# Kernel optimization log

Hardware: AMD Instinct MI355X
Metric: run time of the kernel (lower is better)

Reference implementation:

```python
import jax, jax.numpy as jnp
import numpy as np
import math

N = 100000
E = 3200000
LAMDA = 0.5
ALPHA = 0.1
NLAYERS = 8


def setup_inputs() -> dict:
    key = jax.random.key(0)
    ks = jax.random.split(key, 9)
    x = jax.random.normal(ks[0], (N, 500), dtype=jnp.float32)
    row = jax.random.randint(ks[1], (E,), 0, N, dtype=jnp.int32)
    col = jax.random.randint(ks[2], (E,), 0, N, dtype=jnp.int32)
    # roughly degree-normalized positive edge weights
    edge_weight = jax.random.uniform(ks[3], (E,), dtype=jnp.float32) * (2.0 / 32.0)
    W_in = jax.random.normal(ks[4], (500, 64), dtype=jnp.float32) * (1.0 / math.sqrt(500.0))
    b_in = jnp.zeros((64,), dtype=jnp.float32)
    conv_W = jax.random.normal(ks[5], (NLAYERS, 64, 64), dtype=jnp.float32) * (1.0 / 8.0)
    W_out = jax.random.normal(ks[6], (64, 40), dtype=jnp.float32) * (1.0 / 8.0)
    b_out = jnp.zeros((40,), dtype=jnp.float32)
    return {"x": x, "row": row, "col": col, "edge_weight": edge_weight,
            "W_in": W_in, "b_in": b_in, "conv_W": conv_W,
            "W_out": W_out, "b_out": b_out}


def _spmm(row, col, w, h):
    # adj @ h with adj in COO form: gather source rows, scatter-add to dest
    msgs = h[col] * w[:, None]            # [E, nhidden]
    return jax.ops.segment_sum(msgs, row, num_segments=N)


def reference(x, row, col, edge_weight, W_in, b_in, conv_W, W_out, b_out):
    # dropout is identity in eval mode
    h0 = jax.nn.relu(x @ W_in + b_in)     # [N, nhidden]
    h = h0
    for i in range(NLAYERS):
        l = i + 1
        beta = math.log(LAMDA / l + 1.0)  # identity-mapping strength
        hi = _spmm(row, col, edge_weight, h)
        support = (1.0 - ALPHA) * hi + ALPHA * h0   # initial residual
        h = jax.nn.relu(beta * (support @ conv_W[i]) + (1.0 - beta) * support)
    logits = h @ W_out + b_out
    return jax.nn.log_softmax(logits, axis=1)
```

## Files before the change

### kernel.cpp

```cpp
#include <hip/hip_runtime.h>
#include <math.h>

#define FIN 500
#define NHID 64
#define NCLS 40
#define NLAYERS 8
#define CSHIFT 9
#define CROWS (1 << CSHIFT)
#define PTILE 16384

typedef _Float16 half8 __attribute__((ext_vector_type(8)));
typedef float f32x4 __attribute__((ext_vector_type(4)));

__global__ __launch_bounds__(256) void k_prep(
    const float* __restrict__ Wi, const float* __restrict__ Wc,
    _Float16* __restrict__ WtIn, _Float16* __restrict__ WcT) {
  const int t = blockIdx.x * 256 + threadIdx.x;
  const int stride = gridDim.x * 256;
  for (int i = t; i < 64 * 512; i += stride) {
    int c = i >> 9, k = i & 511;
    WtIn[i] = (k < FIN) ? (_Float16)Wi[k * 64 + c] : (_Float16)0.f;
  }
  for (int i = t; i < NLAYERS * 64 * 64; i += stride) {
    int l = i >> 12, rem = i & 4095, c = rem >> 6, k = rem & 63;
    WcT[i] = (_Float16)Wc[l * 4096 + k * 64 + c];
  }
}

__device__ __forceinline__ half8 load_a_frag(const float* __restrict__ xrow, int gk) {
  half8 a;
  if (gk + 7 < FIN) {
    float4 u = *reinterpret_cast<const float4*>(xrow + gk);
    float4 v = *reinterpret_cast<const float4*>(xrow + gk + 4);
    a[0] = (_Float16)u.x; a[1] = (_Float16)u.y;
    a[2] = (_Float16)u.z; a[3] = (_Float16)u.w;
    a[4] = (_Float16)v.x; a[5] = (_Float16)v.y;
    a[6] = (_Float16)v.z; a[7] = (_Float16)v.w;
  } else {
#pragma unroll
    for (int j = 0; j < 8; ++j)
      a[j] = (gk + j < FIN) ? (_Float16)xrow[gk + j] : (_Float16)0.f;
  }
  return a;
}

__global__ __launch_bounds__(256) void k_gemm_in(
    const float* __restrict__ x, const _Float16* __restrict__ Wt,
    const float* __restrict__ b, _Float16* __restrict__ h0, int n) {
  const int lane = threadIdx.x & 63;
  const int wv = threadIdx.x >> 6;
  const int row0 = blockIdx.x * 64 + wv * 16;
  const int arow = row0 + (lane & 15);
  const int gr = (arow < n) ? arow : (n - 1);
  const int kg = (lane >> 4) * 8;
  const float* xrow = x + (size_t)gr * FIN;
  f32x4 acc[4];
#pragma unroll
  for (int ct = 0; ct < 4; ++ct) acc[ct] = (f32x4){0.f, 0.f, 0.f, 0.f};
  half8 a = load_a_frag(xrow, kg);
#pragma unroll 2
  for (int k0 = 0; k0 < 512; k0 += 32) {
    half8 an = a;
    if (k0 + 32 < 512) an = load_a_frag(xrow, k0 + 32 + kg);
#pragma unroll
    for (int ct = 0; ct < 4; ++ct) {
      const half8 bf = *reinterpret_cast<const half8*>(
          Wt + (size_t)(ct * 16 + (lane & 15)) * 512 + k0 + kg);
      acc[ct] = __builtin_amdgcn_mfma_f32_16x16x32_f16(a, bf, acc[ct], 0, 0, 0);
    }
    a = an;
  }
  const int orow = row0 + (lane >> 4) * 4;
#pragma unroll
  for (int ct = 0; ct < 4; ++ct) {
    const int c = ct * 16 + (lane & 15);
    const float bb = b[c];
#pragma unroll
    for (int i = 0; i < 4; ++i) {
      const int rr = orow + i;
      if (rr < n)
        h0[(size_t)rr * NHID + c] = (_Float16)fmaxf(acc[ct][i] + bb, 0.f);
    }
  }
}

__global__ __launch_bounds__(256) void k_chist(
    const int* __restrict__ row, int* __restrict__ ccnt, int e_total) {
  __shared__ int hist[256];
  const int tid = threadIdx.x;
  hist[tid] = 0;
  __syncthreads();
  const int e0 = blockIdx.x * PTILE;
  for (int t = 0; t < PTILE / 256; ++t) {
    int e = e0 + t * 256 + tid;
    if (e < e_total) atomicAdd(&hist[row[e] >> CSHIFT], 1);
  }
  __syncthreads();
  if (hist[tid]) atomicAdd(&ccnt[tid], hist[tid]);
}

__global__ __launch_bounds__(256) void k_cscan(
    const int* __restrict__ ccnt, int* __restrict__ cbase,
    int* __restrict__ bcur, int* __restrict__ ptr, int nbC, int n, int E) {
  __shared__ int sh[257];
  const int t = threadIdx.x;
  sh[t] = (t < nbC) ? ccnt[t] : 0;
  __syncthreads();
  if (t == 0) {
    int run = 0;
    for (int i = 0; i < 256; ++i) { int v = sh[i]; sh[i] = run; run += v; }
    sh[256] = run;
  }
  __syncthreads();
  if (t <= nbC) cbase[t] = sh[t];
  if (t < nbC) bcur[t] = sh[t];
  if (t == 0) ptr[n] = E;
}

__global__ __launch_bounds__(256) void k_part2(
    const int* __restrict__ row, const int* __restrict__ col,
    const float* __restrict__ w, int* __restrict__ bcurG,
    int2* __restrict__ staged, int e_total, int nbC) {
  __shared__ int hist[256];
  __shared__ int cur[256];
  const int tid = threadIdx.x;
  const int e0 = blockIdx.x * PTILE;
  if (tid < nbC) hist[tid] = 0;
  __syncthreads();
  for (int t = 0; t < PTILE / 256; ++t) {
    int e = e0 + t * 256 + tid;
    if (e < e_total) atomicAdd(&hist[row[e] >> CSHIFT], 1);
  }
  __syncthreads();
  if (tid < nbC) {
    int h = hist[tid];
    cur[tid] = h ? atomicAdd(&bcurG[tid], h) : 0;
  }
  __syncthreads();
  for (int t = 0; t < PTILE / 256; ++t) {
    int e = e0 + t * 256 + tid;
    if (e < e_total) {
      int r = row[e];
      int pos = atomicAdd(&cur[r >> CSHIFT], 1);
      staged[pos] = make_int2(((r & (CROWS - 1)) << 17) | col[e], __float_as_int(w[e]));
    }
  }
}

__global__ __launch_bounds__(256) void k_rebin3(
    const int* __restrict__ cbase, const int2* __restrict__ staged,
    int2* __restrict__ sorted, int* __restrict__ ptr, int n) {
  __shared__ int rcnt[CROWS];
  __shared__ int cur[CROWS];
  __shared__ int wsum[4];
  const int tid = threadIdx.x;
  const int r0 = blockIdx.x << CSHIFT;
  const int bstart = cbase[blockIdx.x], bend = cbase[blockIdx.x + 1];
  rcnt[tid] = 0; rcnt[tid + 256] = 0;
  __syncthreads();
  for (int i = bstart + tid; i < bend; i += 256)
    atomicAdd(&rcnt[staged[i].x >> 17], 1);
  __syncthreads();
  const int lane = tid & 63, wid = tid >> 6;
  int v0 = rcnt[2 * tid], v1 = rcnt[2 * tid + 1];
  int s = v0 + v1;
  int incl = s;
#pragma unroll
  for (int off = 1; off < 64; off <<= 1) {
    int u = __shfl_up(incl, off, 64);
    if (lane >= off) incl += u;
  }
  if (lane == 63) wsum[wid] = incl;
  __syncthreads();
  int woff = 0;
  for (int i = 0; i < wid; ++i) woff += wsum[i];
  int base = bstart + incl - s + woff;
  int rr = r0 + 2 * tid;
  if (rr < n) ptr[rr] = base;
  if (rr + 1 < n) ptr[rr + 1] = base + v0;
  cur[2 * tid] = base;
  cur[2 * tid + 1] = base + v0;
  __syncthreads();
  for (int i = bstart + tid; i < bend; i += 256) {
    int2 e = staged[i];
    int pos = atomicAdd(&cur[e.x >> 17], 1);
    sorted[pos] = make_int2(e.x & 0x1FFFF, e.y);
  }
}

__global__ __launch_bounds__(256) void k_spmm_csr(
    const int* __restrict__ ptr, const int2* __restrict__ sorted,
    const half8* __restrict__ hh, const half8* __restrict__ h0h,
    half8* __restrict__ Sh, int n, int wstride) {
  const int lane = threadIdx.x & 63;
  const int sub = lane >> 3;
  const int fl = lane & 7;
  for (int r = blockIdx.x * 4 + (threadIdx.x >> 6); r < n; r += wstride) {
    const int start = ptr[r], end = ptr[r + 1];
    const half8 h0v = h0h[(size_t)r * 8 + fl];
    float acc[8] = {};
    int e = start + sub;
    for (; e + 24 < end; e += 32) {
      const int2 c0 = sorted[e];
      const int2 c1 = sorted[e + 8];
      const int2 c2 = sorted[e + 16];
      const int2 c3 = sorted[e + 24];
      const half8 v0 = hh[(size_t)c0.x * 8 + fl];
      const half8 v1 = hh[(size_t)c1.x * 8 + fl];
      const half8 v2 = hh[(size_t)c2.x * 8 + fl];
      const half8 v3 = hh[(size_t)c3.x * 8 + fl];
      const float w0 = __int_as_float(c0.y);
      const float w1 = __int_as_float(c1.y);
      const float w2 = __int_as_float(c2.y);
      const float w3 = __int_as_float(c3.y);
#pragma unroll
      for (int j = 0; j < 8; ++j)
        acc[j] += w0 * (float)v0[j] + w1 * (float)v1[j] +
                  w2 * (float)v2[j] + w3 * (float)v3[j];
    }
    for (; e < end; e += 8) {
      const int2 cw = sorted[e];
      const float wv = __int_as_float(cw.y);
      const half8 hv = hh[(size_t)cw.x * 8 + fl];
#pragma unroll
      for (int j = 0; j < 8; ++j) acc[j] += wv * (float)hv[j];
    }
#pragma unroll
    for (int off = 8; off < 64; off <<= 1)
#pragma unroll
      for (int j = 0; j < 8; ++j) acc[j] += __shfl_xor(acc[j], off, 64);
    if (sub == 0) {
      half8 o;
#pragma unroll
      for (int j = 0; j < 8; ++j)
        o[j] = (_Float16)(0.9f * acc[j] + 0.1f * (float)h0v[j]);
      Sh[(size_t)r * 8 + fl] = o;
    }
  }
}

__global__ __launch_bounds__(256) void k_layer(
    const _Float16* __restrict__ Sh, const _Float16* __restrict__ Wt,
    _Float16* __restrict__ hout, float beta, int n) {
  const int lane = threadIdx.x & 63;
  const int wv = threadIdx.x >> 6;
  const int row0 = blockIdx.x * 64 + wv * 16;
  const int arow = row0 + (lane & 15);
  const int gr = (arow < n) ? arow : (n - 1);
  const int kg = (lane >> 4) * 8;
  const half8 a0 = *reinterpret_cast<const half8*>(Sh + (size_t)gr * NHID + kg);
  const half8 a1 = *reinterpret_cast<const half8*>(Sh + (size_t)gr * NHID + 32 + kg);
  f32x4 acc[4];
#pragma unroll
  for (int ct = 0; ct < 4; ++ct) acc[ct] = (f32x4){0.f, 0.f, 0.f, 0.f};
#pragma unroll
  for (int ct = 0; ct < 4; ++ct) {
    const int c = ct * 16 + (lane & 15);
    const half8 b0 = *reinterpret_cast<const half8*>(Wt + c * NHID + kg);
    const half8 b1 = *reinterpret_cast<const half8*>(Wt + c * NHID + 32 + kg);
    acc[ct] = __builtin_amdgcn_mfma_f32_16x16x32_f16(a0, b0, acc[ct], 0, 0, 0);
    acc[ct] = __builtin_amdgcn_mfma_f32_16x16x32_f16(a1, b1, acc[ct], 0, 0, 0);
  }
  const float g = 1.f - beta;
  const int orow = row0 + (lane >> 4) * 4;
#pragma unroll
  for (int ct = 0; ct < 4; ++ct) {
    const int c = ct * 16 + (lane & 15);
#pragma unroll
    for (int i = 0; i < 4; ++i) {
      const int rr = orow + i;
      if (rr < n) {
        const float s = (float)Sh[(size_t)rr * NHID + c];
        hout[(size_t)rr * NHID + c] =
            (_Float16)fmaxf(beta * acc[ct][i] + g * s, 0.f);
      }
    }
  }
}

__global__ __launch_bounds__(256) void k_out(
    const _Float16* __restrict__ h, const float* __restrict__ Wo,
    const float* __restrict__ bo, float* __restrict__ out, int n, int wstride) {
  const int lane = threadIdx.x & 63;
  const int j = (lane < NCLS) ? lane : (NCLS - 1);
  for (int r = blockIdx.x * 4 + (threadIdx.x >> 6); r < n; r += wstride) {
    const float hv = (float)h[(size_t)r * NHID + lane];
    float acc = bo[j];
#pragma unroll 16
    for (int k = 0; k < NHID; ++k) {
      float hk = __shfl(hv, k, 64);
      acc += hk * Wo[k * NCLS + j];
    }
    float v = (lane < NCLS) ? acc : -INFINITY;
    float m = v;
#pragma unroll
    for (int off = 32; off; off >>= 1) m = fmaxf(m, __shfl_xor(m, off, 64));
    float e = (lane < NCLS) ? expf(acc - m) : 0.f;
    float s = e;
#pragma unroll
    for (int off = 32; off; off >>= 1) s += __shfl_xor(s, off, 64);
    if (lane < NCLS) out[(size_t)r * NCLS + lane] = acc - m - logf(s);
  }
}

extern "C" void kernel_launch(void* const* d_in, const int* in_sizes, int n_in,
                              void* d_out, int out_size, void* d_ws, size_t ws_size,
                              hipStream_t stream) {
  const float* x  = (const float*)d_in[0];
  const int* row  = (const int*)d_in[1];
  const int* col  = (const int*)d_in[2];
  const float* ew = (const float*)d_in[3];
  const float* Wi = (const float*)d_in[4];
  const float* bi = (const float*)d_in[5];
  const float* Wc = (const float*)d_in[6];
  const float* Wo = (const float*)d_in[7];
  const float* bo = (const float*)d_in[8];
  float* out = (float*)d_out;

  const int n = in_sizes[0] / FIN;
  const int E = in_sizes[1];

  half8* h0h   = (half8*)d_ws;
  half8* hhA   = h0h + (size_t)n * 8;
  half8* hhB   = hhA + (size_t)n * 8;
  half8* Sh    = hhB + (size_t)n * 8;
  float* A     = (float*)(Sh + (size_t)n * 8);
  int2*  staged= (int2*)A;
  _Float16* WtIn = (_Float16*)A;
  _Float16* WcT  = WtIn + 64 * 512;
  int2*  sorted= (int2*)(A + (size_t)n * NHID);
  int*   ptr   = (int*)(sorted + E);
  int*   ccnt  = ptr + (n + 1);
  int*   cbase = ccnt + 256;
  int*   bcur  = cbase + 257;

  const int nbC = (n + CROWS - 1) >> CSHIFT;
  const int nPB = (E + PTILE - 1) / PTILE;
  dim3 blk(256);

  hipMemsetAsync(ccnt, 0, 256 * sizeof(int), stream);
  k_chist<<<dim3(nPB), blk, 0, stream>>>(row, ccnt, E);
  k_cscan<<<dim3(1), blk, 0, stream>>>(ccnt, cbase, bcur, ptr, nbC, n, E);
  k_part2<<<dim3(nPB), blk, 0, stream>>>(row, col, ew, bcur, staged, E, nbC);
  k_rebin3<<<dim3(nbC), blk, 0, stream>>>(cbase, staged, sorted, ptr, n);

  k_prep<<<dim3(64), blk, 0, stream>>>(Wi, Wc, WtIn, WcT);

  k_gemm_in<<<dim3((n + 63) / 64), blk, 0, stream>>>(x, WtIn, bi, (_Float16*)h0h, n);

  const int spmmBlocks = 2048;
  const half8* hin = h0h;
  for (int l = 0; l < NLAYERS; ++l) {
    half8* hout = (l & 1) ? hhB : hhA;
    k_spmm_csr<<<dim3(spmmBlocks), blk, 0, stream>>>(
        ptr, sorted, hin, h0h, Sh, n, spmmBlocks * 4);
    float beta = logf(0.5f / (float)(l + 1) + 1.f);
    k_layer<<<dim3((n + 63) / 64), blk, 0, stream>>>(
        (const _Float16*)Sh, WcT + (size_t)l * NHID * NHID, (_Float16*)hout, beta, n);
    hin = hout;
  }
  const int outBlocks = 2048;
  k_out<<<dim3(outBlocks), blk, 0, stream>>>(
      (const _Float16*)hin, Wo, bo, out, n, outBlocks * 4);
}
```

Measured before the change: 1.345 ms.

## Fuse SpMM with layer GEMM using column-chunked CSR for cache locality

The edge list is now bucketed by source-column chunk (7 chunks) as well as by destination row block, giving one CSR row-pointer array per chunk. A single fused kernel per layer walks the chunks in turn, accumulates each output row's SpMM result in LDS, adds the initial residual, and runs the MFMA layer transform directly. This removes the intermediate support buffer's global write and read, and the extra kernel launch per layer. It also confines each chunk's gather to a smaller slice of h that is more likely to stay in cache. The cost is that each wave now processes edges one at a time with a scalar fp16 load per lane, instead of eight edges in parallel with vector loads. That adds latency and extra row-pointer reads per chunk.

```diff
diff --git a/kernel.cpp b/kernel.cpp
--- a/kernel.cpp
+++ b/kernel.cpp
@@ -5,9 +5,11 @@
 #define NHID 64
 #define NCLS 40
 #define NLAYERS 8
-#define CSHIFT 9
-#define CROWS (1 << CSHIFT)
 #define PTILE 16384
+#define RSHIFT 12
+#define RROWS 4096
+#define NCHUNK 7
+#define CHSHIFT 14
 
 typedef _Float16 half8 __attribute__((ext_vector_type(8)));
 typedef float f32x4 __attribute__((ext_vector_type(4)));
@@ -85,7 +87,8 @@
 }
 
 __global__ __launch_bounds__(256) void k_chist(
-    const int* __restrict__ row, int* __restrict__ ccnt, int e_total) {
+    const int* __restrict__ row, const int* __restrict__ col,
+    int* __restrict__ ccnt, int e_total, int rh) {
   __shared__ int hist[256];
   const int tid = threadIdx.x;
   hist[tid] = 0;
@@ -93,7 +96,10 @@
   const int e0 = blockIdx.x * PTILE;
   for (int t = 0; t < PTILE / 256; ++t) {
     int e = e0 + t * 256 + tid;
-    if (e < e_total) atomicAdd(&hist[row[e] >> CSHIFT], 1);
+    if (e < e_total) {
+      int ch = col[e] >> CHSHIFT; if (ch > NCHUNK - 1) ch = NCHUNK - 1;
+      atomicAdd(&hist[ch * rh + (row[e] >> RSHIFT)], 1);
+    }
   }
   __syncthreads();
   if (hist[tid]) atomicAdd(&ccnt[tid], hist[tid]);
@@ -101,7 +107,7 @@
 
 __global__ __launch_bounds__(256) void k_cscan(
     const int* __restrict__ ccnt, int* __restrict__ cbase,
-    int* __restrict__ bcur, int* __restrict__ ptr, int nbC, int n, int E) {
+    int* __restrict__ bcur, int nbC) {
   __shared__ int sh[257];
   const int t = threadIdx.x;
   sh[t] = (t < nbC) ? ccnt[t] : 0;
@@ -114,13 +120,12 @@
   __syncthreads();
   if (t <= nbC) cbase[t] = sh[t];
   if (t < nbC) bcur[t] = sh[t];
-  if (t == 0) ptr[n] = E;
 }
 
 __global__ __launch_bounds__(256) void k_part2(
     const int* __restrict__ row, const int* __restrict__ col,
     const float* __restrict__ w, int* __restrict__ bcurG,
-    int2* __restrict__ staged, int e_total, int nbC) {
+    int2* __restrict__ staged, int e_total, int nbC, int rh) {
   __shared__ int hist[256];
   __shared__ int cur[256];
   const int tid = threadIdx.x;
@@ -129,7 +134,10 @@
   __syncthreads();
   for (int t = 0; t < PTILE / 256; ++t) {
     int e = e0 + t * 256 + tid;
-    if (e < e_total) atomicAdd(&hist[row[e] >> CSHIFT], 1);
+    if (e < e_total) {
+      int ch = col[e] >> CHSHIFT; if (ch > NCHUNK - 1) ch = NCHUNK - 1;
+      atomicAdd(&hist[ch * rh + (row[e] >> RSHIFT)], 1);
+    }
   }
   __syncthreads();
   if (tid < nbC) {
@@ -140,30 +148,34 @@
   for (int t = 0; t < PTILE / 256; ++t) {
     int e = e0 + t * 256 + tid;
     if (e < e_total) {
-      int r = row[e];
-      int pos = atomicAdd(&cur[r >> CSHIFT], 1);
-      staged[pos] = make_int2(((r & (CROWS - 1)) << 17) | col[e], __float_as_int(w[e]));
-    }
-  }
-}
-
-__global__ __launch_bounds__(256) void k_rebin3(
+      int r = row[e], c = col[e];
+      int ch = c >> CHSHIFT; if (ch > NCHUNK - 1) ch = NCHUNK - 1;
+      int pos = atomicAdd(&cur[ch * rh + (r >> RSHIFT)], 1);
+      staged[pos] = make_int2(((r & (RROWS - 1)) << 17) | c, __float_as_int(w[e]));
+    }
+  }
+}
+
+__global__ __launch_bounds__(256) void k_rebin4(
     const int* __restrict__ cbase, const int2* __restrict__ staged,
-    int2* __restrict__ sorted, int* __restrict__ ptr, int n) {
-  __shared__ int rcnt[CROWS];
-  __shared__ int cur[CROWS];
+    int2* __restrict__ sorted, int* __restrict__ ptr2, int rh) {
+  __shared__ int rcnt[RROWS];
+  __shared__ int cur[RROWS];
   __shared__ int wsum[4];
   const int tid = threadIdx.x;
-  const int r0 = blockIdx.x << CSHIFT;
+  const int k = blockIdx.x / rh;
+  const int rhigh = blockIdx.x - k * rh;
   const int bstart = cbase[blockIdx.x], bend = cbase[blockIdx.x + 1];
-  rcnt[tid] = 0; rcnt[tid + 256] = 0;
+  for (int i = tid; i < RROWS; i += 256) rcnt[i] = 0;
   __syncthreads();
   for (int i = bstart + tid; i < bend; i += 256)
     atomicAdd(&rcnt[staged[i].x >> 17], 1);
   __syncthreads();
+  const int base = tid * 16;
+  int s = 0;
+#pragma unroll
+  for (int j = 0; j < 16; ++j) s += rcnt[base + j];
   const int lane = tid & 63, wid = tid >> 6;
-  int v0 = rcnt[2 * tid], v1 = rcnt[2 * tid + 1];
-  int s = v0 + v1;
   int incl = s;
 #pragma unroll
   for (int off = 1; off < 64; off <<= 1) {
@@ -174,12 +186,15 @@
   __syncthreads();
   int woff = 0;
   for (int i = 0; i < wid; ++i) woff += wsum[i];
-  int base = bstart + incl - s + woff;
-  int rr = r0 + 2 * tid;
-  if (rr < n) ptr[rr] = base;
-  if (rr + 1 < n) ptr[rr + 1] = base + v0;
-  cur[2 * tid] = base;
-  cur[2 * tid + 1] = base + v0;
+  int run = bstart + (incl - s) + woff;
+  int* p2 = ptr2 + (size_t)k * (rh << RSHIFT) + (rhigh << RSHIFT);
+#pragma unroll
+  for (int j = 0; j < 16; ++j) {
+    int c = rcnt[base + j];
+    p2[base + j] = run;
+    cur[base + j] = run;
+    run += c;
+  }
   __syncthreads();
   for (int i = bstart + tid; i < bend; i += 256) {
     int2 e = staged[i];
@@ -188,91 +203,87 @@
   }
 }
 
-__global__ __launch_bounds__(256) void k_spmm_csr(
-    const int* __restrict__ ptr, const int2* __restrict__ sorted,
-    const half8* __restrict__ hh, const half8* __restrict__ h0h,
-    half8* __restrict__ Sh, int n, int wstride) {
-  const int lane = threadIdx.x & 63;
-  const int sub = lane >> 3;
-  const int fl = lane & 7;
-  for (int r = blockIdx.x * 4 + (threadIdx.x >> 6); r < n; r += wstride) {
-    const int start = ptr[r], end = ptr[r + 1];
-    const half8 h0v = h0h[(size_t)r * 8 + fl];
-    float acc[8] = {};
-    int e = start + sub;
-    for (; e + 24 < end; e += 32) {
-      const int2 c0 = sorted[e];
-      const int2 c1 = sorted[e + 8];
-      const int2 c2 = sorted[e + 16];
-      const int2 c3 = sorted[e + 24];
-      const half8 v0 = hh[(size_t)c0.x * 8 + fl];
-      const half8 v1 = hh[(size_t)c1.x * 8 + fl];
-      const half8 v2 = hh[(size_t)c2.x * 8 + fl];
-      const half8 v3 = hh[(size_t)c3.x * 8 + fl];
-      const float w0 = __int_as_float(c0.y);
-      const float w1 = __int_as_float(c1.y);
-      const float w2 = __int_as_float(c2.y);
-      const float w3 = __int_as_float(c3.y);
-#pragma unroll
-      for (int j = 0; j < 8; ++j)
-        acc[j] += w0 * (float)v0[j] + w1 * (float)v1[j] +
-                  w2 * (float)v2[j] + w3 * (float)v3[j];
-    }
-    for (; e < end; e += 8) {
-      const int2 cw = sorted[e];
-      const float wv = __int_as_float(cw.y);
-      const half8 hv = hh[(size_t)cw.x * 8 + fl];
-#pragma unroll
-      for (int j = 0; j < 8; ++j) acc[j] += wv * (float)hv[j];
-    }
-#pragma unroll
-    for (int off = 8; off < 64; off <<= 1)
-#pragma unroll
-      for (int j = 0; j < 8; ++j) acc[j] += __shfl_xor(acc[j], off, 64);
-    if (sub == 0) {
-      half8 o;
-#pragma unroll
-      for (int j = 0; j < 8; ++j)
-        o[j] = (_Float16)(0.9f * acc[j] + 0.1f * (float)h0v[j]);
-      Sh[(size_t)r * 8 + fl] = o;
-    }
-  }
-}
-
-__global__ __launch_bounds__(256) void k_layer(
-    const _Float16* __restrict__ Sh, const _Float16* __restrict__ Wt,
-    _Float16* __restrict__ hout, float beta, int n) {
-  const int lane = threadIdx.x & 63;
-  const int wv = threadIdx.x >> 6;
-  const int row0 = blockIdx.x * 64 + wv * 16;
-  const int arow = row0 + (lane & 15);
-  const int gr = (arow < n) ? arow : (n - 1);
+__global__ __launch_bounds__(256, 8) void k_fused(
+    const int* __restrict__ ptr2, const int2* __restrict__ sorted,
+    const _Float16* __restrict__ hin, const _Float16* __restrict__ h0,
+    const _Float16* __restrict__ Wt, _Float16* __restrict__ hout,
+    float beta, int n, int s2) {
+  __shared__ float S[64 * 66];
+  const int tid = threadIdx.x;
+  const int lane = tid & 63;
+  const int wid = tid >> 6;
+  const int row0 = blockIdx.x * 64;
+  for (int i = tid; i < 64 * 66; i += 256) S[i] = 0.f;
+  __syncthreads();
+  const int rbase = row0 + wid * 16;
+  const _Float16* hl = hin + lane;
+  for (int k = 0; k < NCHUNK; ++k) {
+    const int* p2 = ptr2 + (size_t)k * s2;
+    int e0 = p2[rbase];
+    for (int rr = 0; rr < 16; ++rr) {
+      const int r = rbase + rr;
+      if (r >= n) break;
+      const int e1 = p2[r + 1];
+      float acc = 0.f;
+      int e = e0;
+      for (; e + 3 < e1; e += 4) {
+        const int2 c0 = sorted[e];
+        const int2 c1 = sorted[e + 1];
+        const int2 c2 = sorted[e + 2];
+        const int2 c3 = sorted[e + 3];
+        const float v0 = (float)hl[(size_t)c0.x * NHID];
+        const float v1 = (float)hl[(size_t)c1.x * NHID];
+        const float v2 = (float)hl[(size_t)c2.x * NHID];
+        const float v3 = (float)hl[(size_t)c3.x * NHID];
+        acc += __int_as_float(c0.y) * v0 + __int_as_float(c1.y) * v1 +
+               __int_as_float(c2.y) * v2 + __int_as_float(c3.y) * v3;
+      }
+      for (; e < e1; ++e) {
+        const int2 cw = sorted[e];
+        acc += __int_as_float(cw.y) * (float)hl[(size_t)cw.x * NHID];
+      }
+      S[(wid * 16 + rr) * 66 + lane] += acc;
+      e0 = e1;
+    }
+  }
+  for (int rr = 0; rr < 16; ++rr) {
+    const int r = rbase + rr;
+    if (r >= n) break;
+    float* sp = &S[(wid * 16 + rr) * 66 + lane];
+    *sp = 0.9f * *sp + 0.1f * (float)h0[(size_t)r * NHID + lane];
+  }
+  __syncthreads();
+  const int al = lane & 15;
   const int kg = (lane >> 4) * 8;
-  const half8 a0 = *reinterpret_cast<const half8*>(Sh + (size_t)gr * NHID + kg);
-  const half8 a1 = *reinterpret_cast<const half8*>(Sh + (size_t)gr * NHID + 32 + kg);
+  const float* sa = &S[(wid * 16 + al) * 66 + kg];
+  half8 a0, a1;
+#pragma unroll
+  for (int j = 0; j < 8; ++j) a0[j] = (_Float16)sa[j];
+#pragma unroll
+  for (int j = 0; j < 8; ++j) a1[j] = (_Float16)sa[32 + j];
   f32x4 acc[4];
 #pragma unroll
   for (int ct = 0; ct < 4; ++ct) acc[ct] = (f32x4){0.f, 0.f, 0.f, 0.f};
 #pragma unroll
   for (int ct = 0; ct < 4; ++ct) {
-    const int c = ct * 16 + (lane & 15);
+    const int c = ct * 16 + al;
     const half8 b0 = *reinterpret_cast<const half8*>(Wt + c * NHID + kg);
     const half8 b1 = *reinterpret_cast<const half8*>(Wt + c * NHID + 32 + kg);
     acc[ct] = __builtin_amdgcn_mfma_f32_16x16x32_f16(a0, b0, acc[ct], 0, 0, 0);
     acc[ct] = __builtin_amdgcn_mfma_f32_16x16x32_f16(a1, b1, acc[ct], 0, 0, 0);
   }
   const float g = 1.f - beta;
-  const int orow = row0 + (lane >> 4) * 4;
+  const int ri = (lane >> 4) * 4;
 #pragma unroll
   for (int ct = 0; ct < 4; ++ct) {
-    const int c = ct * 16 + (lane & 15);
+    const int c = ct * 16 + al;
 #pragma unroll
     for (int i = 0; i < 4; ++i) {
-      const int rr = orow + i;
-      if (rr < n) {
-        const float s = (float)Sh[(size_t)rr * NHID + c];
-        hout[(size_t)rr * NHID + c] =
-            (_Float16)fmaxf(beta * acc[ct][i] + g * s, 0.f);
+      const int r = rbase + ri + i;
+      if (r < n) {
+        const float sv = S[(wid * 16 + ri + i) * 66 + c];
+        hout[(size_t)r * NHID + c] =
+            (_Float16)fmaxf(beta * acc[ct][i] + g * sv, 0.f);
       }
     }
   }
@@ -320,46 +331,44 @@
   const int n = in_sizes[0] / FIN;
   const int E = in_sizes[1];
 
-  half8* h0h   = (half8*)d_ws;
-  half8* hhA   = h0h + (size_t)n * 8;
-  half8* hhB   = hhA + (size_t)n * 8;
-  half8* Sh    = hhB + (size_t)n * 8;
-  float* A     = (float*)(Sh + (size_t)n * 8);
-  int2*  staged= (int2*)A;
-  _Float16* WtIn = (_Float16*)A;
+  const int rh = (n + RROWS - 1) >> RSHIFT;
+  const int s2 = rh << RSHIFT;
+  const int nbC2 = NCHUNK * rh;
+
+  _Float16* h0h = (_Float16*)d_ws;
+  _Float16* hhA = h0h + (size_t)n * NHID;
+  _Float16* hhB = hhA + (size_t)n * NHID;
+  int2* staged  = (int2*)(hhB + (size_t)n * NHID);
+  int2* sorted  = staged + E;
+  int*  ptr2    = (int*)(sorted + E);
+  int*  ccnt    = ptr2 + (size_t)NCHUNK * s2 + 1;
+  int*  cbase   = ccnt + 256;
+  int*  bcur    = cbase + 257;
+  _Float16* WtIn = (_Float16*)(((uintptr_t)(bcur + 256) + 63) & ~(uintptr_t)63);
   _Float16* WcT  = WtIn + 64 * 512;
-  int2*  sorted= (int2*)(A + (size_t)n * NHID);
-  int*   ptr   = (int*)(sorted + E);
-  int*   ccnt  = ptr + (n + 1);
-  int*   cbase = ccnt + 256;
-  int*   bcur  = cbase + 257;
-
-  const int nbC = (n + CROWS - 1) >> CSHIFT;
+
   const int nPB = (E + PTILE - 1) / PTILE;
+  const int nBF = (n + 63) / 64;
   dim3 blk(256);
 
   hipMemsetAsync(ccnt, 0, 256 * sizeof(int), stream);
-  k_chist<<<dim3(nPB), blk, 0, stream>>>(row, ccnt, E);
-  k_cscan<<<dim3(1), blk, 0, stream>>>(ccnt, cbase, bcur, ptr, nbC, n, E);
-  k_part2<<<dim3(nPB), blk, 0, stream>>>(row, col, ew, bcur, staged, E, nbC);
-  k_rebin3<<<dim3(nbC), blk, 0, stream>>>(cbase, staged, sorted, ptr, n);
+  k_chist<<<dim3(nPB), blk, 0, stream>>>(row, col, ccnt, E, rh);
+  k_cscan<<<dim3(1), blk, 0, stream>>>(ccnt, cbase, bcur, nbC2);
+  k_part2<<<dim3(nPB), blk, 0, stream>>>(row, col, ew, bcur, staged, E, nbC2, rh);
+  k_rebin4<<<dim3(nbC2), blk, 0, stream>>>(cbase, staged, sorted, ptr2, rh);
 
   k_prep<<<dim3(64), blk, 0, stream>>>(Wi, Wc, WtIn, WcT);
 
-  k_gemm_in<<<dim3((n + 63) / 64), blk, 0, stream>>>(x, WtIn, bi, (_Float16*)h0h, n);
-
-  const int spmmBlocks = 2048;
-  const half8* hin = h0h;
+  k_gemm_in<<<dim3(nBF), blk, 0, stream>>>(x, WtIn, bi, h0h, n);
+
+  const _Float16* hin = h0h;
   for (int l = 0; l < NLAYERS; ++l) {
-    half8* hout = (l & 1) ? hhB : hhA;
-    k_spmm_csr<<<dim3(spmmBlocks), blk, 0, stream>>>(
-        ptr, sorted, hin, h0h, Sh, n, spmmBlocks * 4);
+    _Float16* hout = (l & 1) ? hhB : hhA;
     float beta = logf(0.5f / (float)(l + 1) + 1.f);
-    k_layer<<<dim3((n + 63) / 64), blk, 0, stream>>>(
-        (const _Float16*)Sh, WcT + (size_t)l * NHID * NHID, (_Float16*)hout, beta, n);
+    k_fused<<<dim3(nBF), blk, 0, stream>>>(
+        ptr2, sorted, hin, h0h, WcT + (size_t)l * NHID * NHID, hout, beta, n, s2);
     hin = hout;
   }
   const int outBlocks = 2048;
-  k_out<<<dim3(outBlocks), blk, 0, stream>>>(
-      (const _Float16*)hin, Wo, bo, out, n, outBlocks * 4);
-}
+  k_out<<<dim3(outBlocks), blk, 0, stream>>>(hin, Wo, bo, out, n, outBlocks * 4);
+}
```

Measured after the change: 2.302 ms. 1.71x slower.
